# Kernel optimization log

Hardware: AMD Instinct MI355X
Metric: run time of the kernel (lower is better)

Reference implementation:

```python
import jax, jax.numpy as jnp
import numpy as np

B, S, D, H, RANK, NC = 2, 2048, 1024, 16, 128, 16
DH = D // H


def setup_inputs() -> dict:
    key = jax.random.key(0)
    ks = jax.random.split(key, 10)
    x = jax.random.normal(ks[0], (B, S, D), jnp.float32)
    # causal mask, broadcast over batch and heads like torch's [B,1,S,S]
    mask = jnp.tril(jnp.ones((S, S), dtype=bool))[None, None]
    # orthogonal-ish init approximated by scaled gaussian
    compress_neurons = jax.random.normal(ks[1], (NC, D, RANK), jnp.float32) / np.sqrt(D)
    router_Q = jax.random.normal(ks[2], (NC, D), jnp.float32) * 0.02
    router_K = jax.random.normal(ks[3], (NC, D), jnp.float32) * 0.02
    router_V = jax.random.normal(ks[4], (NC, D), jnp.float32) * 0.02
    wQ = jax.random.normal(ks[5], (D, RANK), jnp.float32) / np.sqrt(RANK)
    wK = jax.random.normal(ks[6], (D, RANK), jnp.float32) / np.sqrt(RANK)
    wV = jax.random.normal(ks[7], (D, RANK), jnp.float32) / np.sqrt(RANK)
    wO = jax.random.normal(ks[8], (D, D), jnp.float32) / np.sqrt(D)
    return {"x": x, "mask": mask, "compress_neurons": compress_neurons,
            "router_Q": router_Q, "router_K": router_K, "router_V": router_V,
            "wQ": wQ, "wK": wK, "wV": wV, "wO": wO}


def reference(x, mask, compress_neurons, router_Q, router_K, router_V, wQ, wK, wV, wO):
    def compress(router_w):
        # router scores -> softmax over all n_compress neurons
        w = jax.nn.softmax(jnp.einsum('bsd,nd->bsn', x, router_w), axis=-1)  # [B,S,NC]
        # softmax-weighted sum of all neuron projections (fused einsum)
        return jnp.einsum('bsd,ndr,bsn->bsr', x, compress_neurons, w)  # [B,S,RANK]

    hQ = compress(router_Q)
    hK = compress(router_K)
    hV = compress(router_V)
    # expand rank -> d_model (Linear weight [D,RANK]), then split heads
    Q = jnp.einsum('bsr,dr->bsd', hQ, wQ).reshape(B, S, H, DH).transpose(0, 2, 1, 3)
    K = jnp.einsum('bsr,dr->bsd', hK, wK).reshape(B, S, H, DH).transpose(0, 2, 1, 3)
    V = jnp.einsum('bsr,dr->bsd', hV, wV).reshape(B, S, H, DH).transpose(0, 2, 1, 3)
    scores = jnp.einsum('bhqd,bhkd->bhqk', Q, K) / np.sqrt(DH)  # [B,H,S,S]
    scores = jnp.where(mask, scores, -jnp.inf)
    attn = jax.nn.softmax(scores, axis=-1)
    attn_out = jnp.einsum('bhqk,bhkd->bhqd', attn, V)
    attn_out = attn_out.transpose(0, 2, 1, 3).reshape(B, S, D)
    # dropout omitted (eval mode / dropout=0)
    return jnp.einsum('bsd,ed->bse', attn_out, wO)
```

## Files before the change

kernel.cpp:

```cpp
#include <hip/hip_runtime.h>
#include <hip/hip_bf16.h>
#include <math.h>

#define B_ 2
#define S_ 2048
#define D_ 1024
#define H_ 16
#define RANK_ 128
#define NC_ 16
#define DH_ 64
#define T_ (B_*S_)
#define NZ_ 2176

typedef __attribute__((ext_vector_type(8))) __bf16 bf16x8;
typedef __attribute__((ext_vector_type(8))) unsigned short u16x8;
typedef __attribute__((ext_vector_type(4))) float f32x4;
typedef __attribute__((ext_vector_type(16))) float f32x16;

#if __has_builtin(__builtin_amdgcn_exp2f)
#define EXP2F(x) __builtin_amdgcn_exp2f(x)
#else
#define EXP2F(x) exp2f(x)
#endif

__device__ __forceinline__ unsigned short f2bu(float f) {
    __hip_bfloat16 h = __float2bfloat16(f);
    unsigned short u; __builtin_memcpy(&u, &h, 2); return u;
}
__device__ __forceinline__ float bu2f(unsigned short u) {
    __hip_bfloat16 h; __builtin_memcpy(&h, &u, 2); return __bfloat162float(h);
}

__device__ __forceinline__ void gl_lds16(const unsigned short* g, unsigned short* l) {
    __builtin_amdgcn_global_load_lds(
        (const __attribute__((address_space(1))) void*)g,
        (__attribute__((address_space(3))) void*)l, 16, 0, 0);
}

__device__ __forceinline__ unsigned cvtpk_bf16(float lo, float hi) {
    unsigned r;
    asm("v_cvt_pk_bf16_f32 %0, %1, %2" : "=v"(r) : "v"(lo), "v"(hi));
    return r;
}
__device__ __forceinline__ void plswap(unsigned &a, unsigned &b) {
    asm("v_permlane32_swap_b32 %0, %1" : "+v"(a), "+v"(b));
}

__device__ __forceinline__ bool sniff_f32(const unsigned* __restrict__ p) {
    int votes = 0;
    #pragma unroll
    for (int i = 0; i < 64; i++) {
        unsigned e = (p[i] >> 23) & 0xFFu;
        votes += (e >= 0x60u && e <= 0x8Fu) ? 1 : 0;
    }
    return votes >= 32;
}

struct Cvt { const void* src[9]; unsigned short* dst[9]; const void* C; unsigned short* Ct; };

__global__ __launch_bounds__(256) void k_inputs(Cvt cv,
    const unsigned* __restrict__ probe)
{
    bool f32 = sniff_f32(probe);
    if (blockIdx.x < 512) {
        int bid = blockIdx.x;
        int d0 = (bid & 15) * 64, r0 = ((bid >> 4) & 1) * 64, n = bid >> 5;
        __shared__ unsigned short tile[64][65];
        for (int idx = threadIdx.x; idx < 4096; idx += 256) {
            int row = idx >> 6, col = idx & 63;
            size_t si = ((size_t)n*D_ + d0 + row)*RANK_ + r0 + col;
            tile[row][col] = f32 ? f2bu(((const float*)cv.C)[si])
                                 : ((const unsigned short*)cv.C)[si];
        }
        __syncthreads();
        for (int idx = threadIdx.x; idx < 4096; idx += 256) {
            int row = idx >> 6, col = idx & 63;
            cv.Ct[((size_t)(n*RANK_ + r0 + row))*D_ + d0 + col] = tile[col][row];
        }
        return;
    }
    const int offs[9] = {0, 4194304, 4210688, 4227072, 4243456,
                         4259840, 4390912, 4521984, 4653056};
    const int total = 5701632;
    int nconv = gridDim.x - 512;
    int stride = nconv * 256;
    for (int i = (blockIdx.x - 512) * 256 + threadIdx.x; i < total; i += stride) {
        int seg = 0;
        #pragma unroll
        for (int s = 1; s < 9; s++) seg += (i >= offs[s]) ? 1 : 0;
        int local = i - offs[seg];
        const void* sp = cv.src[seg];
        unsigned short v = 0;
        if (sp) v = f32 ? f2bu(((const float*)sp)[local]) : ((const unsigned short*)sp)[local];
        cv.dst[seg][local] = v;
    }
}

template<int MT, int MODE>
__global__ __launch_bounds__(256) void k_mfma_gemm(const unsigned short* __restrict__ A,
    const unsigned short* __restrict__ Bm, void* __restrict__ Cout,
    const unsigned* __restrict__ probe, int M, int N, int K)
{
    bool f32out = false;
    if (MODE == 2) f32out = sniff_f32(probe);
    __shared__ __align__(16) unsigned short As[MT*32*32];
    __shared__ __align__(16) unsigned short Bs[128*32];
    const int tid = threadIdx.x;
    const int wv = tid >> 6, lane = tid & 63;
    const int wm = (wv >> 1) * (MT*16), wn = (wv & 1) * 64;
    const int quad = lane >> 4, l16 = lane & 15;
    const int m0 = blockIdx.x * (MT*32), n0 = blockIdx.y * 128;

    const f32x4 z4 = {0.f, 0.f, 0.f, 0.f};
    f32x4 acc[MT][4];
    #pragma unroll
    for (int i = 0; i < MT; i++)
        #pragma unroll
        for (int j = 0; j < 4; j++) acc[i][j] = z4;

    for (int k0 = 0; k0 < K; k0 += 32) {
        __syncthreads();
        #pragma unroll
        for (int c = 0; c < MT/2; c++) {
            int idx = wv*64 + c*256 + lane;
            gl_lds16(A + (size_t)(m0 + (idx >> 2))*K + k0 + (idx & 3)*8,
                     &As[(wv*64 + c*256)*8]);
        }
        #pragma unroll
        for (int c = 0; c < 2; c++) {
            int idx = wv*64 + c*256 + lane;
            gl_lds16(Bm + (size_t)(n0 + (idx >> 2))*K + k0 + (idx & 3)*8,
                     &Bs[(wv*64 + c*256)*8]);
        }
        __syncthreads();
        bf16x8 af[MT], bfr[4];
        #pragma unroll
        for (int mt = 0; mt < MT; mt++) af[mt]  = *(const bf16x8*)&As[(wm + mt*16 + l16)*32 + quad*8];
        #pragma unroll
        for (int nt = 0; nt < 4; nt++) bfr[nt] = *(const bf16x8*)&Bs[(wn + nt*16 + l16)*32 + quad*8];
        #pragma unroll
        for (int mt = 0; mt < MT; mt++)
            #pragma unroll
            for (int nt = 0; nt < 4; nt++)
                acc[mt][nt] = __builtin_amdgcn_mfma_f32_16x16x32_bf16(af[mt], bfr[nt], acc[mt][nt], 0, 0, 0);
    }
    #pragma unroll
    for (int mt = 0; mt < MT; mt++)
        #pragma unroll
        for (int nt = 0; nt < 4; nt++) {
            int col = n0 + wn + nt*16 + l16;
            #pragma unroll
            for (int r = 0; r < 4; r++) {
                int rowg = m0 + wm + mt*16 + quad*4 + r;
                float v = acc[mt][nt][r];
                if (MODE == 2 && f32out) ((float*)Cout)[(size_t)rowg*N + col] = v;
                else  ((unsigned short*)Cout)[(size_t)rowg*N + col] = f2bu(v);
            }
        }
}

__global__ __launch_bounds__(256) void k_qkv2(const unsigned short* __restrict__ h3,
    const unsigned short* __restrict__ wqkv, unsigned short* __restrict__ QKb,
    unsigned short* __restrict__ Vtg)
{
    __shared__ __align__(16) unsigned short As[128*32];
    __shared__ __align__(16) unsigned short Bs[128*32];
    const int tid = threadIdx.x;
    const int wv = tid >> 6, lane = tid & 63;
    const int wm = (wv >> 1) * 64, wn = (wv & 1) * 64;
    const int quad = lane >> 4, l16 = lane & 15;

    const bool vt = (blockIdx.x >= 512);
    int m0, n0;
    const unsigned short *A, *Bm;
    float scale = 1.f;
    if (!vt) {
        int id = blockIdx.x;
        m0 = (id & 31) * 128;
        n0 = (id >> 5) * 128;
        int w = n0 >> 10;
        A  = h3 + (size_t)w * T_ * RANK_ + (size_t)m0 * RANK_;
        Bm = wqkv + (size_t)w * D_ * RANK_ + (size_t)(n0 & 1023) * RANK_;
        if (w == 0) scale = 0.125f * 1.44269504f;
    } else {
        int id = blockIdx.x - 512;
        m0 = (id & 7) * 128;
        n0 = (id >> 3) * 128;
        A  = wqkv + (size_t)2 * D_ * RANK_ + (size_t)m0 * RANK_;
        Bm = h3 + (size_t)2 * T_ * RANK_ + (size_t)n0 * RANK_;
    }

    const f32x4 z4 = {0.f, 0.f, 0.f, 0.f};
    f32x4 acc[4][4];
    #pragma unroll
    for (int i = 0; i < 4; i++)
        #pragma unroll
        for (int j = 0; j < 4; j++) acc[i][j] = z4;

    for (int k0 = 0; k0 < RANK_; k0 += 32) {
        __syncthreads();
        #pragma unroll
        for (int c = 0; c < 2; c++) {
            int idx = wv*64 + c*256 + lane;
            gl_lds16(A  + (size_t)(idx >> 2)*RANK_ + k0 + (idx & 3)*8,
                     &As[(wv*64 + c*256)*8]);
            gl_lds16(Bm + (size_t)(idx >> 2)*RANK_ + k0 + (idx & 3)*8,
                     &Bs[(wv*64 + c*256)*8]);
        }
        __syncthreads();
        bf16x8 af[4], bfr[4];
        #pragma unroll
        for (int mt = 0; mt < 4; mt++) af[mt]  = *(const bf16x8*)&As[(wm + mt*16 + l16)*32 + quad*8];
        #pragma unroll
        for (int nt = 0; nt < 4; nt++) bfr[nt] = *(const bf16x8*)&Bs[(wn + nt*16 + l16)*32 + quad*8];
        #pragma unroll
        for (int mt = 0; mt < 4; mt++)
            #pragma unroll
            for (int nt = 0; nt < 4; nt++)
                acc[mt][nt] = __builtin_amdgcn_mfma_f32_16x16x32_bf16(af[mt], bfr[nt], acc[mt][nt], 0, 0, 0);
    }
    #pragma unroll
    for (int mt = 0; mt < 4; mt++)
        #pragma unroll
        for (int nt = 0; nt < 4; nt++) {
            #pragma unroll
            for (int r = 0; r < 4; r++) {
                int rowg = m0 + wm + mt*16 + quad*4 + r;
                int col  = n0 + wn + nt*16 + l16;
                float v = acc[mt][nt][r] * scale;
                if (!vt) {
                    QKb[(size_t)(col >> 10)*T_*D_ + (size_t)rowg*D_ + (col & 1023)]
                        = f2bu(v);
                } else {
                    size_t vrow = (size_t)((col >> 11)*H_ + (rowg >> 6))*64 + (rowg & 63);
                    Vtg[vrow*S_ + (col & 2047)] = f2bu(v);
                }
            }
        }
}

__global__ __launch_bounds__(256) void k_hreduce(const unsigned short* __restrict__ z,
    unsigned short* __restrict__ h)
{
    int t0 = blockIdx.x * 2;
    int tg = threadIdx.x >> 7, r = threadIdx.x & 127;
    int t = t0 + tg;
    __shared__ float sc[2][48];
    __shared__ float wl[2][3][16];
    if (threadIdx.x < 96) {
        int tk = threadIdx.x / 48, j = threadIdx.x % 48;
        sc[tk][j] = bu2f(z[(size_t)(t0 + tk)*NZ_ + 2048 + j]);
    }
    __syncthreads();
    if (threadIdx.x < 6) {
        int tk = threadIdx.x / 3, w = threadIdx.x % 3;
        float m = -INFINITY;
        for (int n = 0; n < 16; n++) m = fmaxf(m, sc[tk][w*16 + n]);
        float s = 0.f, e[16];
        for (int n = 0; n < 16; n++) { e[n] = __expf(sc[tk][w*16 + n] - m); s += e[n]; }
        float inv = 1.f / s;
        for (int n = 0; n < 16; n++) wl[tk][w][n] = e[n] * inv;
    }
    __syncthreads();
    const unsigned short* zr = z + (size_t)t * NZ_;
    float acc[3] = {0.f, 0.f, 0.f};
    #pragma unroll
    for (int n = 0; n < NC_; n++) {
        float zv = bu2f(zr[n*RANK_ + r]);
        #pragma unroll
        for (int w = 0; w < 3; w++) acc[w] += wl[tg][w][n] * zv;
    }
    #pragma unroll
    for (int w = 0; w < 3; w++) h[((size_t)w*T_ + t)*RANK_ + r] = f2bu(acc[w]);
}

__global__ __launch_bounds__(256, 1) void k_flash_mfma(const unsigned short* __restrict__ Qm,
    const unsigned short* __restrict__ Km, const unsigned short* __restrict__ Vtg,
    unsigned short* __restrict__ Om)
{
    const int qt = blockIdx.x;
    const int hh = blockIdx.y, b = blockIdx.z;
    __shared__ __align__(16) unsigned short Ks[4][64*64];
    __shared__ __align__(16) unsigned short Vs[4][64*64];
    const int tid = threadIdx.x;
    const int w = tid >> 6, lane = tid & 63;
    const int l32 = lane & 31, hi = lane >> 5;
    const size_t base  = ((size_t)b * S_) * D_ + (size_t)hh * DH_;
    const size_t vbase = (size_t)((b*H_ + hh) * 64) * S_;
    const int tok0 = qt*256 + w*64;

    bf16x8 aq[2][4];
    #pragma unroll
    for (int tq = 0; tq < 2; tq++)
        #pragma unroll
        for (int ks = 0; ks < 4; ks++)
            aq[tq][ks] = *(const bf16x8*)(Qm + base +
                (size_t)(tok0 + tq*32 + l32)*D_ + ks*16 + hi*8);

    const int nkt = 4*(qt + 1);

    auto STAGE = [&](int kt_, int bf_) {
        #pragma unroll
        for (int c = 0; c < 2; c++) {
            int idx = c*256 + tid;
            int row = idx >> 3, j = (idx & 7) ^ (row & 7);
            gl_lds16(Km + base + (size_t)(kt_*64 + row)*D_ + j*8,
                     &Ks[bf_][(c*256 + (w<<6))*8]);
        }
        #pragma unroll
        for (int c = 0; c < 2; c++) {
            int idx = c*256 + tid;
            int row = idx >> 3, j = (idx & 7) ^ (row & 7);
            gl_lds16(Vtg + vbase + (size_t)row*S_ + kt_*64 + j*8,
                     &Vs[bf_][(c*256 + (w<<6))*8]);
        }
    };

    STAGE(0, 0); STAGE(1, 1); STAGE(2, 2);

    f32x16 oacc[2][2];
    #pragma unroll
    for (int tq = 0; tq < 2; tq++)
        #pragma unroll
        for (int db = 0; db < 2; db++)
            #pragma unroll
            for (int i = 0; i < 16; i++) oacc[tq][db][i] = 0.f;
    float ls[2][4];
    #pragma unroll
    for (int tq = 0; tq < 2; tq++)
        #pragma unroll
        for (int j = 0; j < 4; j++) ls[tq][j] = 0.f;

    for (int kt = 0; kt < nkt; kt++) {
        const int cur = kt & 3;
        const int rem = nkt - 1 - kt;
        if (rem >= 2)      asm volatile("s_waitcnt vmcnt(8)" ::: "memory");
        else if (rem == 1) asm volatile("s_waitcnt vmcnt(4)" ::: "memory");
        else               asm volatile("s_waitcnt vmcnt(0)" ::: "memory");
        __builtin_amdgcn_s_barrier();
        __builtin_amdgcn_sched_barrier(0);

        if (kt + 3 < nkt) STAGE(kt + 3, (kt + 3) & 3);

        f32x16 sacc[2][2];
        #pragma unroll
        for (int tq = 0; tq < 2; tq++)
            #pragma unroll
            for (int kb = 0; kb < 2; kb++)
                #pragma unroll
                for (int i = 0; i < 16; i++) sacc[tq][kb][i] = 0.f;
        #pragma unroll
        for (int ks = 0; ks < 4; ks++)
            #pragma unroll
            for (int kb = 0; kb < 2; kb++) {
                int row = kb*32 + l32;
                int c = (ks*2 + hi) ^ (row & 7);
                bf16x8 ak = *(const bf16x8*)&Ks[cur][row*64 + c*8];
                sacc[0][kb] = __builtin_amdgcn_mfma_f32_32x32x16_bf16(ak, aq[0][ks], sacc[0][kb], 0, 0, 0);
                sacc[1][kb] = __builtin_amdgcn_mfma_f32_32x32x16_bf16(ak, aq[1][ks], sacc[1][kb], 0, 0, 0);
            }

        if (kt >= 4*qt) {
            #pragma unroll
            for (int tq = 0; tq < 2; tq++) {
                int tokg = tok0 + tq*32 + l32;
                #pragma unroll
                for (int kb = 0; kb < 2; kb++)
                    #pragma unroll
                    for (int r = 0; r < 16; r++) {
                        int keyg = kt*64 + kb*32 + (r&3) + 8*(r>>2) + 4*hi;
                        if (keyg > tokg) sacc[tq][kb][r] = -INFINITY;
                    }
            }
        }

        bf16x8 pa[2][4];
        #pragma unroll
        for (int tq = 0; tq < 2; tq++)
            #pragma unroll
            for (int kb = 0; kb < 2; kb++) {
                float pv[16];
                #pragma unroll
                for (int r = 0; r < 16; r++) {
                    pv[r] = EXP2F(sacc[tq][kb][r]);
                    ls[tq][r & 3] += pv[r];
                }
                unsigned wd[8];
                #pragma unroll
                for (int j = 0; j < 8; j++) wd[j] = cvtpk_bf16(pv[2*j], pv[2*j+1]);
                plswap(wd[0], wd[2]); plswap(wd[1], wd[3]);
                plswap(wd[4], wd[6]); plswap(wd[5], wd[7]);
                union { unsigned u[4]; bf16x8 v; } u0, u1;
                u0.u[0]=wd[0]; u0.u[1]=wd[1]; u0.u[2]=wd[2]; u0.u[3]=wd[3];
                u1.u[0]=wd[4]; u1.u[1]=wd[5]; u1.u[2]=wd[6]; u1.u[3]=wd[7];
                pa[tq][2*kb]   = u0.v;
                pa[tq][2*kb+1] = u1.v;
            }

        #pragma unroll
        for (int ks = 0; ks < 4; ks++)
            #pragma unroll
            for (int db = 0; db < 2; db++) {
                int row = db*32 + l32;
                int c = (ks*2 + hi) ^ (row & 7);
                bf16x8 bv = *(const bf16x8*)&Vs[cur][row*64 + c*8];
                oacc[0][db] = __builtin_amdgcn_mfma_f32_32x32x16_bf16(pa[0][ks], bv, oacc[0][db], 0, 0, 0);
                oacc[1][db] = __builtin_amdgcn_mfma_f32_32x32x16_bf16(pa[1][ks], bv, oacc[1][db], 0, 0, 0);
            }
    }

    #pragma unroll
    for (int tq = 0; tq < 2; tq++) {
        float l = (ls[tq][0] + ls[tq][1]) + (ls[tq][2] + ls[tq][3]);
        l += __shfl_xor(l, 32);
        float inv = 1.f / l;
        #pragma unroll
        for (int r = 0; r < 16; r++) {
            int crow = (r&3) + 8*(r>>2) + 4*hi;
            float invr = __shfl(inv, crow);
            size_t rowo = base + (size_t)(tok0 + tq*32 + crow)*D_;
            #pragma unroll
            for (int db = 0; db < 2; db++)
                Om[rowo + db*32 + l32] = f2bu(oacc[tq][db][r] * invr);
        }
    }
}

extern "C" void kernel_launch(void* const* d_in, const int* in_sizes, int n_in,
                              void* d_out, int out_size, void* d_ws, size_t ws_size,
                              hipStream_t stream)
{
    const unsigned* probe = (const unsigned*)d_in[0];

    unsigned short* u = (unsigned short*)d_ws;
    unsigned short* xc   = u;               size_t o = (size_t)T_*D_;
    unsigned short* wqkv = u + o;           o += (size_t)3*D_*RANK_;
    unsigned short* wOc  = u + o;           o += (size_t)D_*D_;
    unsigned short* Ct   = u + o;           o += (size_t)NZ_*D_;
    unsigned short* h3   = u + o;           o += (size_t)3*T_*RANK_;
    unsigned short* QKb  = u + o;           o += (size_t)2*T_*D_;
    unsigned short* Vtg  = u + o;           o += (size_t)T_*D_;
    unsigned short* z    = u + o;           o += (size_t)T_*NZ_;
    unsigned short* attnb= u + o;           o += (size_t)T_*D_;

    unsigned short* Rp = Ct + (size_t)2048*D_;
    unsigned short* Qb = QKb;
    unsigned short* Kb = QKb + (size_t)T_*D_;

    Cvt cv;
    cv.src[0] = d_in[0]; cv.dst[0] = xc;
    cv.src[1] = d_in[3]; cv.dst[1] = Rp;
    cv.src[2] = d_in[4]; cv.dst[2] = Rp + 16384;
    cv.src[3] = d_in[5]; cv.dst[3] = Rp + 32768;
    cv.src[4] = nullptr; cv.dst[4] = Rp + 49152;
    cv.src[5] = d_in[6]; cv.dst[5] = wqkv;
    cv.src[6] = d_in[7]; cv.dst[6] = wqkv + 131072;
    cv.src[7] = d_in[8]; cv.dst[7] = wqkv + 262144;
    cv.src[8] = d_in[9]; cv.dst[8] = wOc;
    cv.C = d_in[2]; cv.Ct = Ct;
    k_inputs<<<512 + 2048, 256, 0, stream>>>(cv, probe);

    k_mfma_gemm<4,0><<<dim3(T_/128, NZ_/128), 256, 0, stream>>>(
        xc, Ct, z, nullptr, T_, NZ_, D_);

    k_hreduce<<<T_/2, 256, 0, stream>>>(z, h3);

    k_qkv2<<<768, 256, 0, stream>>>(h3, wqkv, QKb, Vtg);

    k_flash_mfma<<<dim3(8, H_, B_), 256, 0, stream>>>(Qb, Kb, Vtg, attnb);

    k_mfma_gemm<2,2><<<dim3(T_/64, D_/128), 256, 0, stream>>>(
        attnb, wOc, d_out, probe, T_, D_, D_);
}
```

Baseline: 255.2 us.

## Split flash attention into single-wave blocks with heavy-first causal scheduling

Restructures the flash attention kernel so each block is one 64-lane wave handling 64 query rows. It uses 32-key tiles with a 3-stage LDS ring, which removes the workgroup barrier and gives 1024 blocks instead of 256. Block indices are remapped so the longest causal query tiles launch first, to balance load across CUs. In exchange, each K/V tile is loaded by more blocks with no cross-wave sharing, and an lgkmcnt wait is added before each refill.

```diff
diff --git a/kernel.cpp b/kernel.cpp
--- a/kernel.cpp
+++ b/kernel.cpp
@@ -274,20 +274,22 @@
     for (int w = 0; w < 3; w++) h[((size_t)w*T_ + t)*RANK_ + r] = f2bu(acc[w]);
 }
 
-__global__ __launch_bounds__(256, 1) void k_flash_mfma(const unsigned short* __restrict__ Qm,
+__global__ __launch_bounds__(64) void k_flash_mfma(const unsigned short* __restrict__ Qm,
     const unsigned short* __restrict__ Km, const unsigned short* __restrict__ Vtg,
     unsigned short* __restrict__ Om)
 {
-    const int qt = blockIdx.x;
-    const int hh = blockIdx.y, b = blockIdx.z;
-    __shared__ __align__(16) unsigned short Ks[4][64*64];
-    __shared__ __align__(16) unsigned short Vs[4][64*64];
-    const int tid = threadIdx.x;
-    const int w = tid >> 6, lane = tid & 63;
+    const int x = blockIdx.x;
+    const int gr = (x & 7) | ((x >> 8) << 3);
+    const int qt = 31 - ((x >> 3) & 31);
+    const int hh = gr & 15, b = gr >> 4;
+
+    __shared__ __align__(16) unsigned short Ks[3][32*64];
+    __shared__ __align__(16) unsigned short Vs[3][64*32];
+    const int lane = threadIdx.x & 63;
     const int l32 = lane & 31, hi = lane >> 5;
     const size_t base  = ((size_t)b * S_) * D_ + (size_t)hh * DH_;
     const size_t vbase = (size_t)((b*H_ + hh) * 64) * S_;
-    const int tok0 = qt*256 + w*64;
+    const int tok0 = qt * 64;
 
     bf16x8 aq[2][4];
     #pragma unroll
@@ -297,26 +299,28 @@
             aq[tq][ks] = *(const bf16x8*)(Qm + base +
                 (size_t)(tok0 + tq*32 + l32)*D_ + ks*16 + hi*8);
 
-    const int nkt = 4*(qt + 1);
+    const int nkt = 2*(qt + 1);
 
     auto STAGE = [&](int kt_, int bf_) {
         #pragma unroll
-        for (int c = 0; c < 2; c++) {
-            int idx = c*256 + tid;
+        for (int c = 0; c < 4; c++) {
+            int idx = c*64 + lane;
             int row = idx >> 3, j = (idx & 7) ^ (row & 7);
-            gl_lds16(Km + base + (size_t)(kt_*64 + row)*D_ + j*8,
-                     &Ks[bf_][(c*256 + (w<<6))*8]);
-        }
-        #pragma unroll
-        for (int c = 0; c < 2; c++) {
-            int idx = c*256 + tid;
-            int row = idx >> 3, j = (idx & 7) ^ (row & 7);
-            gl_lds16(Vtg + vbase + (size_t)row*S_ + kt_*64 + j*8,
-                     &Vs[bf_][(c*256 + (w<<6))*8]);
+            gl_lds16(Km + base + (size_t)(kt_*32 + row)*D_ + j*8,
+                     &Ks[bf_][c*64*8]);
+        }
+        #pragma unroll
+        for (int c = 0; c < 4; c++) {
+            int idx = c*64 + lane;
+            int row = idx >> 2, j = (idx & 3) ^ (row & 3);
+            gl_lds16(Vtg + vbase + (size_t)row*S_ + kt_*32 + j*8,
+                     &Vs[bf_][c*64*8]);
         }
     };
 
-    STAGE(0, 0); STAGE(1, 1); STAGE(2, 2);
+    STAGE(0, 0);
+    STAGE(1, 1);
+    if (nkt > 2) STAGE(2, 2);
 
     f32x16 oacc[2][2];
     #pragma unroll
@@ -332,81 +336,75 @@
         for (int j = 0; j < 4; j++) ls[tq][j] = 0.f;
 
     for (int kt = 0; kt < nkt; kt++) {
-        const int cur = kt & 3;
+        const int cur = kt % 3;
         const int rem = nkt - 1 - kt;
-        if (rem >= 2)      asm volatile("s_waitcnt vmcnt(8)" ::: "memory");
-        else if (rem == 1) asm volatile("s_waitcnt vmcnt(4)" ::: "memory");
+        if (rem >= 2)      asm volatile("s_waitcnt vmcnt(16)" ::: "memory");
+        else if (rem == 1) asm volatile("s_waitcnt vmcnt(8)" ::: "memory");
         else               asm volatile("s_waitcnt vmcnt(0)" ::: "memory");
-        __builtin_amdgcn_s_barrier();
         __builtin_amdgcn_sched_barrier(0);
 
-        if (kt + 3 < nkt) STAGE(kt + 3, (kt + 3) & 3);
-
-        f32x16 sacc[2][2];
+        f32x16 sacc[2];
         #pragma unroll
         for (int tq = 0; tq < 2; tq++)
             #pragma unroll
-            for (int kb = 0; kb < 2; kb++)
-                #pragma unroll
-                for (int i = 0; i < 16; i++) sacc[tq][kb][i] = 0.f;
-        #pragma unroll
-        for (int ks = 0; ks < 4; ks++)
-            #pragma unroll
-            for (int kb = 0; kb < 2; kb++) {
-                int row = kb*32 + l32;
-                int c = (ks*2 + hi) ^ (row & 7);
-                bf16x8 ak = *(const bf16x8*)&Ks[cur][row*64 + c*8];
-                sacc[0][kb] = __builtin_amdgcn_mfma_f32_32x32x16_bf16(ak, aq[0][ks], sacc[0][kb], 0, 0, 0);
-                sacc[1][kb] = __builtin_amdgcn_mfma_f32_32x32x16_bf16(ak, aq[1][ks], sacc[1][kb], 0, 0, 0);
-            }
-
-        if (kt >= 4*qt) {
+            for (int i = 0; i < 16; i++) sacc[tq][i] = 0.f;
+        #pragma unroll
+        for (int ks = 0; ks < 4; ks++) {
+            int c = (ks*2 + hi) ^ (l32 & 7);
+            bf16x8 ak = *(const bf16x8*)&Ks[cur][l32*64 + c*8];
+            sacc[0] = __builtin_amdgcn_mfma_f32_32x32x16_bf16(ak, aq[0][ks], sacc[0], 0, 0, 0);
+            sacc[1] = __builtin_amdgcn_mfma_f32_32x32x16_bf16(ak, aq[1][ks], sacc[1], 0, 0, 0);
+        }
+
+        if (kt >= 2*qt) {
             #pragma unroll
             for (int tq = 0; tq < 2; tq++) {
                 int tokg = tok0 + tq*32 + l32;
                 #pragma unroll
-                for (int kb = 0; kb < 2; kb++)
-                    #pragma unroll
-                    for (int r = 0; r < 16; r++) {
-                        int keyg = kt*64 + kb*32 + (r&3) + 8*(r>>2) + 4*hi;
-                        if (keyg > tokg) sacc[tq][kb][r] = -INFINITY;
-                    }
+                for (int r = 0; r < 16; r++) {
+                    int keyg = kt*32 + (r&3) + 8*(r>>2) + 4*hi;
+                    if (keyg > tokg) sacc[tq][r] = -INFINITY;
+                }
             }
         }
 
-        bf16x8 pa[2][4];
-        #pragma unroll
-        for (int tq = 0; tq < 2; tq++)
-            #pragma unroll
-            for (int kb = 0; kb < 2; kb++) {
-                float pv[16];
-                #pragma unroll
-                for (int r = 0; r < 16; r++) {
-                    pv[r] = EXP2F(sacc[tq][kb][r]);
-                    ls[tq][r & 3] += pv[r];
-                }
-                unsigned wd[8];
-                #pragma unroll
-                for (int j = 0; j < 8; j++) wd[j] = cvtpk_bf16(pv[2*j], pv[2*j+1]);
-                plswap(wd[0], wd[2]); plswap(wd[1], wd[3]);
-                plswap(wd[4], wd[6]); plswap(wd[5], wd[7]);
-                union { unsigned u[4]; bf16x8 v; } u0, u1;
-                u0.u[0]=wd[0]; u0.u[1]=wd[1]; u0.u[2]=wd[2]; u0.u[3]=wd[3];
-                u1.u[0]=wd[4]; u1.u[1]=wd[5]; u1.u[2]=wd[6]; u1.u[3]=wd[7];
-                pa[tq][2*kb]   = u0.v;
-                pa[tq][2*kb+1] = u1.v;
+        bf16x8 pa[2][2];
+        #pragma unroll
+        for (int tq = 0; tq < 2; tq++) {
+            float pv[16];
+            #pragma unroll
+            for (int r = 0; r < 16; r++) {
+                pv[r] = EXP2F(sacc[tq][r]);
+                ls[tq][r & 3] += pv[r];
             }
-
-        #pragma unroll
-        for (int ks = 0; ks < 4; ks++)
+            unsigned wd[8];
+            #pragma unroll
+            for (int j = 0; j < 8; j++) wd[j] = cvtpk_bf16(pv[2*j], pv[2*j+1]);
+            plswap(wd[0], wd[2]); plswap(wd[1], wd[3]);
+            plswap(wd[4], wd[6]); plswap(wd[5], wd[7]);
+            union { unsigned u[4]; bf16x8 v; } u0, u1;
+            u0.u[0]=wd[0]; u0.u[1]=wd[1]; u0.u[2]=wd[2]; u0.u[3]=wd[3];
+            u1.u[0]=wd[4]; u1.u[1]=wd[5]; u1.u[2]=wd[6]; u1.u[3]=wd[7];
+            pa[tq][0] = u0.v;
+            pa[tq][1] = u1.v;
+        }
+
+        #pragma unroll
+        for (int ks = 0; ks < 2; ks++)
             #pragma unroll
             for (int db = 0; db < 2; db++) {
                 int row = db*32 + l32;
-                int c = (ks*2 + hi) ^ (row & 7);
-                bf16x8 bv = *(const bf16x8*)&Vs[cur][row*64 + c*8];
+                int c = (ks*2 + hi) ^ (row & 3);
+                bf16x8 bv = *(const bf16x8*)&Vs[cur][row*32 + c*8];
                 oacc[0][db] = __builtin_amdgcn_mfma_f32_32x32x16_bf16(pa[0][ks], bv, oacc[0][db], 0, 0, 0);
                 oacc[1][db] = __builtin_amdgcn_mfma_f32_32x32x16_bf16(pa[1][ks], bv, oacc[1][db], 0, 0, 0);
             }
+
+        if (kt + 3 < nkt) {
+            asm volatile("s_waitcnt lgkmcnt(0)" ::: "memory");
+            __builtin_amdgcn_sched_barrier(0);
+            STAGE(kt + 3, cur);
+        }
     }
 
     #pragma unroll
@@ -467,7 +465,7 @@
 
     k_qkv2<<<768, 256, 0, stream>>>(h3, wqkv, QKb, Vtg);
 
-    k_flash_mfma<<<dim3(8, H_, B_), 256, 0, stream>>>(Qb, Kb, Vtg, attnb);
+    k_flash_mfma<<<dim3(1024), 64, 0, stream>>>(Qb, Kb, Vtg, attnb);
 
     k_mfma_gemm<2,2><<<dim3(T_/64, D_/128), 256, 0, stream>>>(
         attnb, wOc, d_out, probe, T_, D_, D_);
```

After: 272.3 us. 1.07x slower.

## Split flash attention into 128-query blocks with load-balanced heavy-first ordering

Applied to the files above, without the earlier changes.

The flash attention kernel now uses 128-thread blocks covering 128 queries each, launching 512 blocks instead of 256. Block indices are remapped so the causal tiles with the most key blocks are scheduled first in one half of the grid and the lightest in the other. The 4-deep asynchronous K/V staging pipeline with explicit vmcnt waits is replaced by a simple double buffer with __syncthreads. The aim is more parallelism and better causal load balance across CUs, but each key tile is now loaded by twice as many blocks and less load latency is hidden.

```diff
diff --git a/kernel.cpp b/kernel.cpp
--- a/kernel.cpp
+++ b/kernel.cpp
@@ -274,20 +274,24 @@
     for (int w = 0; w < 3; w++) h[((size_t)w*T_ + t)*RANK_ + r] = f2bu(acc[w]);
 }
 
-__global__ __launch_bounds__(256, 1) void k_flash_mfma(const unsigned short* __restrict__ Qm,
+__global__ __launch_bounds__(128) void k_flash_mfma(const unsigned short* __restrict__ Qm,
     const unsigned short* __restrict__ Km, const unsigned short* __restrict__ Vtg,
     unsigned short* __restrict__ Om)
 {
-    const int qt = blockIdx.x;
-    const int hh = blockIdx.y, b = blockIdx.z;
-    __shared__ __align__(16) unsigned short Ks[4][64*64];
-    __shared__ __align__(16) unsigned short Vs[4][64*64];
+    const int i = blockIdx.x;
+    const int half = i >> 8, r_ = i & 255;
+    const int gr = r_ & 31, ts = r_ >> 5;
+    const int qt = half ? ts : (15 - ts);
+    const int hh = gr & 15, b = gr >> 4;
+
+    __shared__ __align__(16) unsigned short Ks[2][64*64];
+    __shared__ __align__(16) unsigned short Vs[2][64*64];
     const int tid = threadIdx.x;
     const int w = tid >> 6, lane = tid & 63;
     const int l32 = lane & 31, hi = lane >> 5;
     const size_t base  = ((size_t)b * S_) * D_ + (size_t)hh * DH_;
     const size_t vbase = (size_t)((b*H_ + hh) * 64) * S_;
-    const int tok0 = qt*256 + w*64;
+    const int tok0 = qt*128 + w*64;
 
     bf16x8 aq[2][4];
     #pragma unroll
@@ -297,50 +301,54 @@
             aq[tq][ks] = *(const bf16x8*)(Qm + base +
                 (size_t)(tok0 + tq*32 + l32)*D_ + ks*16 + hi*8);
 
-    const int nkt = 4*(qt + 1);
-
-    auto STAGE = [&](int kt_, int bf_) {
-        #pragma unroll
-        for (int c = 0; c < 2; c++) {
-            int idx = c*256 + tid;
-            int row = idx >> 3, j = (idx & 7) ^ (row & 7);
-            gl_lds16(Km + base + (size_t)(kt_*64 + row)*D_ + j*8,
-                     &Ks[bf_][(c*256 + (w<<6))*8]);
-        }
-        #pragma unroll
-        for (int c = 0; c < 2; c++) {
-            int idx = c*256 + tid;
-            int row = idx >> 3, j = (idx & 7) ^ (row & 7);
-            gl_lds16(Vtg + vbase + (size_t)row*S_ + kt_*64 + j*8,
-                     &Vs[bf_][(c*256 + (w<<6))*8]);
-        }
-    };
-
-    STAGE(0, 0); STAGE(1, 1); STAGE(2, 2);
-
     f32x16 oacc[2][2];
     #pragma unroll
     for (int tq = 0; tq < 2; tq++)
         #pragma unroll
         for (int db = 0; db < 2; db++)
             #pragma unroll
-            for (int i = 0; i < 16; i++) oacc[tq][db][i] = 0.f;
+            for (int ii = 0; ii < 16; ii++) oacc[tq][db][ii] = 0.f;
     float ls[2][4];
     #pragma unroll
     for (int tq = 0; tq < 2; tq++)
         #pragma unroll
         for (int j = 0; j < 4; j++) ls[tq][j] = 0.f;
 
+    const int nkt = 2*(qt + 1);
+
+    #pragma unroll
+    for (int c = 0; c < 4; c++) {
+        int idx = c*128 + tid;
+        int row = idx >> 3, j = (idx & 7) ^ (row & 7);
+        gl_lds16(Km + base + (size_t)row*D_ + j*8, &Ks[0][(c*128 + (w<<6))*8]);
+    }
+    #pragma unroll
+    for (int c = 0; c < 4; c++) {
+        int idx = c*128 + tid;
+        int row = idx >> 3, j = (idx & 7) ^ (row & 7);
+        gl_lds16(Vtg + vbase + (size_t)row*S_ + j*8, &Vs[0][(c*128 + (w<<6))*8]);
+    }
+
     for (int kt = 0; kt < nkt; kt++) {
-        const int cur = kt & 3;
-        const int rem = nkt - 1 - kt;
-        if (rem >= 2)      asm volatile("s_waitcnt vmcnt(8)" ::: "memory");
-        else if (rem == 1) asm volatile("s_waitcnt vmcnt(4)" ::: "memory");
-        else               asm volatile("s_waitcnt vmcnt(0)" ::: "memory");
-        __builtin_amdgcn_s_barrier();
-        __builtin_amdgcn_sched_barrier(0);
-
-        if (kt + 3 < nkt) STAGE(kt + 3, (kt + 3) & 3);
+        const int cur = kt & 1;
+        __syncthreads();
+
+        if (kt + 1 < nkt) {
+            #pragma unroll
+            for (int c = 0; c < 4; c++) {
+                int idx = c*128 + tid;
+                int row = idx >> 3, j = (idx & 7) ^ (row & 7);
+                gl_lds16(Km + base + (size_t)((kt+1)*64 + row)*D_ + j*8,
+                         &Ks[1-cur][(c*128 + (w<<6))*8]);
+            }
+            #pragma unroll
+            for (int c = 0; c < 4; c++) {
+                int idx = c*128 + tid;
+                int row = idx >> 3, j = (idx & 7) ^ (row & 7);
+                gl_lds16(Vtg + vbase + (size_t)row*S_ + (kt+1)*64 + j*8,
+                         &Vs[1-cur][(c*128 + (w<<6))*8]);
+            }
+        }
 
         f32x16 sacc[2][2];
         #pragma unroll
@@ -348,7 +356,7 @@
             #pragma unroll
             for (int kb = 0; kb < 2; kb++)
                 #pragma unroll
-                for (int i = 0; i < 16; i++) sacc[tq][kb][i] = 0.f;
+                for (int ii = 0; ii < 16; ii++) sacc[tq][kb][ii] = 0.f;
         #pragma unroll
         for (int ks = 0; ks < 4; ks++)
             #pragma unroll
@@ -360,7 +368,7 @@
                 sacc[1][kb] = __builtin_amdgcn_mfma_f32_32x32x16_bf16(ak, aq[1][ks], sacc[1][kb], 0, 0, 0);
             }
 
-        if (kt >= 4*qt) {
+        if (kt >= 2*qt) {
             #pragma unroll
             for (int tq = 0; tq < 2; tq++) {
                 int tokg = tok0 + tq*32 + l32;
@@ -467,7 +475,7 @@
 
     k_qkv2<<<768, 256, 0, stream>>>(h3, wqkv, QKb, Vtg);
 
-    k_flash_mfma<<<dim3(8, H_, B_), 256, 0, stream>>>(Qb, Kb, Vtg, attnb);
+    k_flash_mfma<<<dim3(512), 128, 0, stream>>>(Qb, Kb, Vtg, attnb);
 
     k_mfma_gemm<2,2><<<dim3(T_/64, D_/128), 256, 0, stream>>>(
         attnb, wOc, d_out, probe, T_, D_, D_);
```

After: 250.8 us. Within noise of the previous version (-1.7%).
